# Kernel tuning notes

Hardware: AMD Instinct MI355X
Metric: run time of the kernel (lower is better)

Reference implementation:

```python
import jax, jax.numpy as jnp
import numpy as np

N_NODES = 1536
IN_FEATURES = 1433
N_HIDDEN = 64      # total across 8 heads -> 8 per head
N_HEADS = 8
N_CLASSES = 7
NEG_SLOPE = 0.2    # LeakyReLU slope in GATv2 layer


def setup_inputs() -> dict:
    key = jax.random.key(0)
    k_x, k_adj, k_w1, k_a1, k_w2, k_a2 = jax.random.split(key, 6)
    x = jax.random.normal(k_x, (N_NODES, IN_FEATURES), dtype=jnp.float32)
    adj = jax.random.uniform(k_adj, (N_NODES, N_NODES)) < 0.01
    adj = adj | jnp.eye(N_NODES, dtype=bool)
    adj_mat = adj[:, :, None]  # [n, n, 1]
    # layer 1 (share_weights=True -> one linear for l and r), attn vector shared across heads
    s1 = 1.0 / np.sqrt(IN_FEATURES)
    W1 = jax.random.uniform(k_w1, (IN_FEATURES, N_HIDDEN), minval=-s1, maxval=s1, dtype=jnp.float32)
    a1 = jax.random.uniform(k_a1, (N_HIDDEN // N_HEADS,), minval=-1.0, maxval=1.0, dtype=jnp.float32)
    # layer 2: 1 head, n_classes features, is_concat=False (mean over the single head)
    s2 = 1.0 / np.sqrt(N_HIDDEN)
    W2 = jax.random.uniform(k_w2, (N_HIDDEN, N_CLASSES), minval=-s2, maxval=s2, dtype=jnp.float32)
    a2 = jax.random.uniform(k_a2, (N_CLASSES,), minval=-1.0, maxval=1.0, dtype=jnp.float32)
    return {"x": x, "adj_mat": adj_mat, "W1": W1, "a1": a1, "W2": W2, "a2": a2}


def _gatv2_layer(h, adj, W, a, n_heads, is_concat):
    n = h.shape[0]
    g = (h @ W).reshape(n, n_heads, -1)              # shared weights: g_l == g_r == g
    # pairwise scores: e[i,j,h] = a . leaky_relu(g[j] + g[i])  (symmetric since weights shared)
    s = jax.nn.leaky_relu(g[:, None] + g[None, :], NEG_SLOPE)   # [n, n, heads, f]
    e = jnp.einsum('ijhf,f->ijh', s, a)                          # [n, n, heads]
    e = jnp.where(adj, e, -jnp.inf)                              # adj broadcasts [n,n,1]
    att = jax.nn.softmax(e, axis=1)                              # softmax over source nodes j
    out = jnp.einsum('ijh,jhf->ihf', att, g)                     # [n, heads, f]
    if is_concat:
        return out.reshape(n, -1)
    return out.mean(axis=1)


def reference(x, adj_mat, W1, a1, W2, a2):
    # dropout layers are identity in eval mode
    h = _gatv2_layer(x, adj_mat, W1, a1, N_HEADS, True)   # [n, n_hidden]
    h = jax.nn.elu(h)
    return _gatv2_layer(h, adj_mat, W2, a2, 1, False)     # [n, n_classes]
```

## Files before the change

### kernel.cpp

```cpp
#include <hip/hip_runtime.h>

#define N_NODES 1536
#define IN_F    1433
#define HID     64
#define NH      8
#define HF      8
#define NC      7
#define MAXN    64
#define GST     66
#define G1_BLOCKS 384
#define ROWS    4
#define XS_STRIDE 1440

__device__ __forceinline__ float waveAllMax(float v) {
#pragma unroll
    for (int o = 32; o > 0; o >>= 1) v = fmaxf(v, __shfl_xor(v, o, 64));
    return v;
}
__device__ __forceinline__ float waveAllSum(float v) {
#pragma unroll
    for (int o = 32; o > 0; o >>= 1) v += __shfl_xor(v, o, 64);
    return v;
}

__global__ __launch_bounds__(256) void k_front(const float* __restrict__ x,
                                               const float* __restrict__ W1,
                                               const unsigned int* __restrict__ adj,
                                               float* __restrict__ g1,
                                               int* __restrict__ cnt,
                                               int* __restrict__ nbr) {
    __shared__ float xs[ROWS * XS_STRIDE];
    __shared__ float red[4 * 256];
    __shared__ int lc;
    const int t = threadIdx.x;

    if (blockIdx.x < G1_BLOCKS) {
        const int i0 = blockIdx.x * ROWS;
        for (int r = 0; r < ROWS; ++r) {
            const float* xr = x + (size_t)(i0 + r) * IN_F;
            for (int k = t; k < XS_STRIDE; k += 256)
                xs[r * XS_STRIDE + k] = (k < IN_F) ? xr[k] : 0.f;
        }
        __syncthreads();
        const int j = t & 63, q = t >> 6;
        float acc[ROWS] = {0.f, 0.f, 0.f, 0.f};
        const int k0 = q * 360;
        for (int kb = k0; kb < k0 + 360; kb += 4) {
            float w[4];
#pragma unroll
            for (int u = 0; u < 4; ++u) {
                int k = kb + u;
                int kc = (k < IN_F) ? k : (IN_F - 1);
                w[u] = W1[(size_t)kc * HID + j];
            }
#pragma unroll
            for (int r = 0; r < ROWS; ++r) {
                float4 xv = *(const float4*)(xs + r * XS_STRIDE + kb);
                acc[r] += xv.x * w[0] + xv.y * w[1] + xv.z * w[2] + xv.w * w[3];
            }
        }
#pragma unroll
        for (int r = 0; r < ROWS; ++r) red[q * 256 + r * 64 + j] = acc[r];
        __syncthreads();
        float s = red[0 * 256 + t] + red[1 * 256 + t] + red[2 * 256 + t] + red[3 * 256 + t];
        g1[(size_t)(i0 + (t >> 6)) * HID + (t & 63)] = s;
    } else {
        const int i = blockIdx.x - G1_BLOCKS;
        if (t == 0) lc = 0;
        __syncthreads();
        const unsigned int* row = adj + (size_t)i * N_NODES;
        for (int j = t; j < N_NODES; j += 256) {
            if (row[j] != 0u) {
                int p = atomicAdd(&lc, 1);
                if (p < MAXN) nbr[i * MAXN + p] = j;
            }
        }
        __syncthreads();
        if (t == 0) {
            int n = (lc > MAXN) ? MAXN : lc;
            if (n == 0) { nbr[i * MAXN] = i; n = 1; }
            cnt[i] = n;
        }
    }
}

__global__ __launch_bounds__(64) void k_attn1(const float* __restrict__ g1,
                                              const int* __restrict__ cnt,
                                              const int* __restrict__ nbr,
                                              const float* __restrict__ a1,
                                              float* __restrict__ h1) {
    __shared__ float gis[HID];
    __shared__ float gj[MAXN * GST];
    __shared__ float es[NH * GST];
    const int i = blockIdx.x, t = threadIdx.x;
    const int n = cnt[i];

    gis[t] = g1[(size_t)i * HID + t];
    const int jn = nbr[i * MAXN + t];
    for (int l = 0; l < n; ++l) {
        int j = __shfl(jn, l, 64);
        gj[l * GST + t] = g1[(size_t)j * HID + t];
    }
    __syncthreads();

    float av[HF];
#pragma unroll
    for (int f = 0; f < HF; ++f) av[f] = a1[f];

    float sc[NH];
    if (t < n) {
#pragma unroll
        for (int h = 0; h < NH; ++h) {
            float s = 0.f;
#pragma unroll
            for (int f = 0; f < HF; ++f) {
                float v = gis[h * HF + f] + gj[t * GST + h * HF + f];
                v = (v >= 0.f) ? v : 0.2f * v;
                s += av[f] * v;
            }
            sc[h] = s;
        }
    } else {
#pragma unroll
        for (int h = 0; h < NH; ++h) sc[h] = -INFINITY;
    }

    float S[NH];
#pragma unroll
    for (int h = 0; h < NH; ++h) {
        float m = waveAllMax(sc[h]);
        float p = (t < n) ? __expf(sc[h] - m) : 0.f;
        es[h * GST + t] = p;
        S[h] = waveAllSum(p);
    }
    __syncthreads();

    const int h = t >> 3;
    float acc = 0.f;
    for (int l = 0; l < n; ++l)
        acc += es[h * GST + l] * gj[l * GST + t];
    acc /= S[h];
    h1[(size_t)i * HID + t] = (acc > 0.f) ? acc : (__expf(acc) - 1.f);
}

__global__ __launch_bounds__(64) void k_back(const float* __restrict__ h1,
                                             const float* __restrict__ W2,
                                             const float* __restrict__ a2,
                                             const int* __restrict__ cnt,
                                             const int* __restrict__ nbr,
                                             float* __restrict__ out) {
    __shared__ float hj[MAXN * GST];
    __shared__ float w2s[HID * NC];
    __shared__ float g2s[MAXN * 8];
    __shared__ float ps[MAXN];
    const int i = blockIdx.x, t = threadIdx.x;
    const int n = cnt[i];

    for (int k = t; k < HID * NC; k += 64) w2s[k] = W2[k];
    const int jn = nbr[i * MAXN + t];
    for (int l = 0; l < n; ++l) {
        int j = __shfl(jn, l, 64);
        hj[l * GST + t] = h1[(size_t)j * HID + t];
    }
    __syncthreads();

    if (t < n) {
#pragma unroll
        for (int c = 0; c < NC; ++c) {
            float s = 0.f;
            for (int f = 0; f < HID; ++f)
                s += hj[t * GST + f] * w2s[f * NC + c];
            g2s[t * 8 + c] = s;
        }
    }
    unsigned long long bal = __ballot(t < n && jn == i);
    int ls = (bal != 0ull) ? (__ffsll((long long)bal) - 1) : 0;
    __syncthreads();

    float scv;
    if (t < n) {
        float s = 0.f;
#pragma unroll
        for (int c = 0; c < NC; ++c) {
            float v = g2s[ls * 8 + c] + g2s[t * 8 + c];
            v = (v >= 0.f) ? v : 0.2f * v;
            s += a2[c] * v;
        }
        scv = s;
    } else scv = -INFINITY;

    float m = waveAllMax(scv);
    float p = (t < n) ? __expf(scv - m) : 0.f;
    ps[t] = p;
    float S = waveAllSum(p);
    __syncthreads();

    if (t < NC) {
        float acc = 0.f;
        for (int l = 0; l < n; ++l)
            acc += ps[l] * g2s[l * 8 + t];
        out[(size_t)i * NC + t] = acc / S;
    }
}

extern "C" void kernel_launch(void* const* d_in, const int* in_sizes, int n_in,
                              void* d_out, int out_size, void* d_ws, size_t ws_size,
                              hipStream_t stream) {
    (void)out_size; (void)ws_size;
    const void* px = nullptr; const void* padj = nullptr;
    const void* pW1 = nullptr; const void* pa1 = nullptr;
    const void* pW2 = nullptr; const void* pa2 = nullptr;
    for (int i = 0; i < n_in; ++i) {
        switch (in_sizes[i]) {
            case N_NODES * IN_F:    px   = d_in[i]; break;
            case N_NODES * N_NODES: padj = d_in[i]; break;
            case IN_F * HID:        pW1  = d_in[i]; break;
            case HF:                pa1  = d_in[i]; break;
            case HID * NC:          pW2  = d_in[i]; break;
            case NC:                pa2  = d_in[i]; break;
            default: break;
        }
    }
    if (!px && n_in > 0)   px   = d_in[0];
    if (!padj && n_in > 1) padj = d_in[1];
    if (!pW1 && n_in > 2)  pW1  = d_in[2];
    if (!pa1 && n_in > 3)  pa1  = d_in[3];
    if (!pW2 && n_in > 4)  pW2  = d_in[4];
    if (!pa2 && n_in > 5)  pa2  = d_in[5];

    char* w = (char*)d_ws;
    size_t off = 0;
    auto carve = [&](size_t bytes) -> char* {
        off = (off + 255) & ~(size_t)255;
        char* p = w + off; off += bytes; return p;
    };
    int*   cnt = (int*)  carve((size_t)N_NODES * 4);
    int*   nbr = (int*)  carve((size_t)N_NODES * MAXN * 4);
    float* g1  = (float*)carve((size_t)N_NODES * HID * 4);
    float* h1  = (float*)carve((size_t)N_NODES * HID * 4);

    float* outp = (float*)d_out;

    k_front<<<G1_BLOCKS + N_NODES, 256, 0, stream>>>((const float*)px, (const float*)pW1,
                                                     (const unsigned int*)padj, g1, cnt, nbr);
    k_attn1<<<N_NODES, 64, 0, stream>>>(g1, cnt, nbr, (const float*)pa1, h1);
    k_back<<<N_NODES, 64, 0, stream>>>(h1, (const float*)pW2, (const float*)pa2,
                                       cnt, nbr, outp);
}
```

Baseline: 122.7 us.

## Fuse three kernels into one cooperative persistent kernel with grid syncs

Merges the GEMM/compaction, layer-1 attention and layer-2 stages into a single cooperative kernel of 512 blocks that loops over work units and separates the stages with grid-wide barriers. Four wavefronts per block each handle one node in the attention stages, using slices of one shared LDS buffer. The aim is to remove two kernel launch gaps and their tail effects. In exchange, the grid-wide barriers add cost, a large LDS allocation limits occupancy, and the host now queries device attributes and occupancy on every call. The old three-kernel path stays as a fallback.

```diff
diff --git a/kernel.cpp b/kernel.cpp
--- a/kernel.cpp
+++ b/kernel.cpp
@@ -1,4 +1,7 @@
 #include <hip/hip_runtime.h>
+#include <hip/hip_cooperative_groups.h>
+
+namespace cg = cooperative_groups;
 
 #define N_NODES 1536
 #define IN_F    1433
@@ -11,6 +14,7 @@
 #define G1_BLOCKS 384
 #define ROWS    4
 #define XS_STRIDE 1440
+#define COOP_GRID 512
 
 __device__ __forceinline__ float waveAllMax(float v) {
 #pragma unroll
@@ -22,6 +26,180 @@
     for (int o = 32; o > 0; o >>= 1) v += __shfl_xor(v, o, 64);
     return v;
 }
+
+
+__device__ __forceinline__ void gemm1_unit(int u, const float* __restrict__ x,
+                                           const float* __restrict__ W1,
+                                           float* __restrict__ g1,
+                                           float* xs, float* red) {
+    const int t = threadIdx.x;
+    const int i0 = u * ROWS;
+    for (int r = 0; r < ROWS; ++r) {
+        const float* xr = x + (size_t)(i0 + r) * IN_F;
+        for (int k = t; k < XS_STRIDE; k += 256)
+            xs[r * XS_STRIDE + k] = (k < IN_F) ? xr[k] : 0.f;
+    }
+    __syncthreads();
+    const int j = t & 63, q = t >> 6;
+    float acc[ROWS] = {0.f, 0.f, 0.f, 0.f};
+    const int k0 = q * 360;
+    for (int kb = k0; kb < k0 + 360; kb += 4) {
+        float w[4];
+#pragma unroll
+        for (int u2 = 0; u2 < 4; ++u2) {
+            int k = kb + u2;
+            int kc = (k < IN_F) ? k : (IN_F - 1);
+            w[u2] = W1[(size_t)kc * HID + j];
+        }
+#pragma unroll
+        for (int r = 0; r < ROWS; ++r) {
+            float4 xv = *(const float4*)(xs + r * XS_STRIDE + kb);
+            acc[r] += xv.x * w[0] + xv.y * w[1] + xv.z * w[2] + xv.w * w[3];
+        }
+    }
+#pragma unroll
+    for (int r = 0; r < ROWS; ++r) red[q * 256 + r * 64 + j] = acc[r];
+    __syncthreads();
+    float s = red[0 * 256 + t] + red[1 * 256 + t] + red[2 * 256 + t] + red[3 * 256 + t];
+    g1[(size_t)(i0 + (t >> 6)) * HID + (t & 63)] = s;
+}
+
+__device__ __forceinline__ void compact_unit(int i, const unsigned int* __restrict__ adj,
+                                             int* __restrict__ cnt, int* __restrict__ nbr,
+                                             int* lc) {
+    const int t = threadIdx.x;
+    if (t == 0) *lc = 0;
+    __syncthreads();
+    const unsigned int* row = adj + (size_t)i * N_NODES;
+    for (int j = t; j < N_NODES; j += 256) {
+        if (row[j] != 0u) {
+            int p = atomicAdd(lc, 1);
+            if (p < MAXN) nbr[i * MAXN + p] = j;
+        }
+    }
+    __syncthreads();
+    if (t == 0) {
+        int n = (*lc > MAXN) ? MAXN : *lc;
+        if (n == 0) { nbr[i * MAXN] = i; n = 1; }
+        cnt[i] = n;
+    }
+}
+
+__device__ __forceinline__ void attn1_node(int i, int lane, const float* __restrict__ g1,
+                                           const int* __restrict__ cnt,
+                                           const int* __restrict__ nbr,
+                                           const float* __restrict__ a1,
+                                           float* __restrict__ h1, float* P) {
+    float* gis = P;
+    float* gj  = P + 64;
+    float* es  = P + 64 + MAXN * GST;
+    const int n = cnt[i];
+
+    gis[lane] = g1[(size_t)i * HID + lane];
+    const int jn = nbr[i * MAXN + lane];
+    for (int l = 0; l < n; ++l) {
+        int j = __shfl(jn, l, 64);
+        gj[l * GST + lane] = g1[(size_t)j * HID + lane];
+    }
+    __syncthreads();
+
+    float av[HF];
+#pragma unroll
+    for (int f = 0; f < HF; ++f) av[f] = a1[f];
+
+    float sc[NH];
+    if (lane < n) {
+#pragma unroll
+        for (int h = 0; h < NH; ++h) {
+            float s = 0.f;
+#pragma unroll
+            for (int f = 0; f < HF; ++f) {
+                float v = gis[h * HF + f] + gj[lane * GST + h * HF + f];
+                v = (v >= 0.f) ? v : 0.2f * v;
+                s += av[f] * v;
+            }
+            sc[h] = s;
+        }
+    } else {
+#pragma unroll
+        for (int h = 0; h < NH; ++h) sc[h] = -INFINITY;
+    }
+
+    float S[NH];
+#pragma unroll
+    for (int h = 0; h < NH; ++h) {
+        float m = waveAllMax(sc[h]);
+        float p = (lane < n) ? __expf(sc[h] - m) : 0.f;
+        es[h * GST + lane] = p;
+        S[h] = waveAllSum(p);
+    }
+    __syncthreads();
+
+    const int h = lane >> 3;
+    float acc = 0.f;
+    for (int l = 0; l < n; ++l)
+        acc += es[h * GST + l] * gj[l * GST + lane];
+    acc /= S[h];
+    h1[(size_t)i * HID + lane] = (acc > 0.f) ? acc : (__expf(acc) - 1.f);
+}
+
+__device__ __forceinline__ void back_node(int i, int lane, const float* __restrict__ h1,
+                                          const float* __restrict__ a2,
+                                          const int* __restrict__ cnt,
+                                          const int* __restrict__ nbr,
+                                          float* __restrict__ out,
+                                          float* Q, const float* w2s) {
+    float* hj  = Q;
+    float* g2s = Q + MAXN * GST;
+    float* ps  = Q + MAXN * GST + MAXN * 8;
+    const int n = cnt[i];
+
+    const int jn = nbr[i * MAXN + lane];
+    for (int l = 0; l < n; ++l) {
+        int j = __shfl(jn, l, 64);
+        hj[l * GST + lane] = h1[(size_t)j * HID + lane];
+    }
+    __syncthreads();
+
+    if (lane < n) {
+#pragma unroll
+        for (int c = 0; c < NC; ++c) {
+            float s = 0.f;
+            for (int f = 0; f < HID; ++f)
+                s += hj[lane * GST + f] * w2s[f * NC + c];
+            g2s[lane * 8 + c] = s;
+        }
+    }
+    unsigned long long bal = __ballot(lane < n && jn == i);
+    int ls = (bal != 0ull) ? (__ffsll((long long)bal) - 1) : 0;
+    __syncthreads();
+
+    float scv;
+    if (lane < n) {
+        float s = 0.f;
+#pragma unroll
+        for (int c = 0; c < NC; ++c) {
+            float v = g2s[ls * 8 + c] + g2s[lane * 8 + c];
+            v = (v >= 0.f) ? v : 0.2f * v;
+            s += a2[c] * v;
+        }
+        scv = s;
+    } else scv = -INFINITY;
+
+    float m = waveAllMax(scv);
+    float p = (lane < n) ? __expf(scv - m) : 0.f;
+    ps[lane] = p;
+    float S = waveAllSum(p);
+    __syncthreads();
+
+    if (lane < NC) {
+        float acc = 0.f;
+        for (int l = 0; l < n; ++l)
+            acc += ps[l] * g2s[l * 8 + lane];
+        out[(size_t)i * NC + lane] = acc / S;
+    }
+}
+
 
 __global__ __launch_bounds__(256) void k_front(const float* __restrict__ x,
                                                const float* __restrict__ W1,
@@ -32,56 +210,8 @@
     __shared__ float xs[ROWS * XS_STRIDE];
     __shared__ float red[4 * 256];
     __shared__ int lc;
-    const int t = threadIdx.x;
-
-    if (blockIdx.x < G1_BLOCKS) {
-        const int i0 = blockIdx.x * ROWS;
-        for (int r = 0; r < ROWS; ++r) {
-            const float* xr = x + (size_t)(i0 + r) * IN_F;
-            for (int k = t; k < XS_STRIDE; k += 256)
-                xs[r * XS_STRIDE + k] = (k < IN_F) ? xr[k] : 0.f;
-        }
-        __syncthreads();
-        const int j = t & 63, q = t >> 6;
-        float acc[ROWS] = {0.f, 0.f, 0.f, 0.f};
-        const int k0 = q * 360;
-        for (int kb = k0; kb < k0 + 360; kb += 4) {
-            float w[4];
-#pragma unroll
-            for (int u = 0; u < 4; ++u) {
-                int k = kb + u;
-                int kc = (k < IN_F) ? k : (IN_F - 1);
-                w[u] = W1[(size_t)kc * HID + j];
-            }
-#pragma unroll
-            for (int r = 0; r < ROWS; ++r) {
-                float4 xv = *(const float4*)(xs + r * XS_STRIDE + kb);
-                acc[r] += xv.x * w[0] + xv.y * w[1] + xv.z * w[2] + xv.w * w[3];
-            }
-        }
-#pragma unroll
-        for (int r = 0; r < ROWS; ++r) red[q * 256 + r * 64 + j] = acc[r];
-        __syncthreads();
-        float s = red[0 * 256 + t] + red[1 * 256 + t] + red[2 * 256 + t] + red[3 * 256 + t];
-        g1[(size_t)(i0 + (t >> 6)) * HID + (t & 63)] = s;
-    } else {
-        const int i = blockIdx.x - G1_BLOCKS;
-        if (t == 0) lc = 0;
-        __syncthreads();
-        const unsigned int* row = adj + (size_t)i * N_NODES;
-        for (int j = t; j < N_NODES; j += 256) {
-            if (row[j] != 0u) {
-                int p = atomicAdd(&lc, 1);
-                if (p < MAXN) nbr[i * MAXN + p] = j;
-            }
-        }
-        __syncthreads();
-        if (t == 0) {
-            int n = (lc > MAXN) ? MAXN : lc;
-            if (n == 0) { nbr[i * MAXN] = i; n = 1; }
-            cnt[i] = n;
-        }
-    }
+    if (blockIdx.x < G1_BLOCKS) gemm1_unit(blockIdx.x, x, W1, g1, xs, red);
+    else                        compact_unit(blockIdx.x - G1_BLOCKS, adj, cnt, nbr, &lc);
 }
 
 __global__ __launch_bounds__(64) void k_attn1(const float* __restrict__ g1,
@@ -89,58 +219,8 @@
                                               const int* __restrict__ nbr,
                                               const float* __restrict__ a1,
                                               float* __restrict__ h1) {
-    __shared__ float gis[HID];
-    __shared__ float gj[MAXN * GST];
-    __shared__ float es[NH * GST];
-    const int i = blockIdx.x, t = threadIdx.x;
-    const int n = cnt[i];
-
-    gis[t] = g1[(size_t)i * HID + t];
-    const int jn = nbr[i * MAXN + t];
-    for (int l = 0; l < n; ++l) {
-        int j = __shfl(jn, l, 64);
-        gj[l * GST + t] = g1[(size_t)j * HID + t];
-    }
-    __syncthreads();
-
-    float av[HF];
-#pragma unroll
-    for (int f = 0; f < HF; ++f) av[f] = a1[f];
-
-    float sc[NH];
-    if (t < n) {
-#pragma unroll
-        for (int h = 0; h < NH; ++h) {
-            float s = 0.f;
-#pragma unroll
-            for (int f = 0; f < HF; ++f) {
-                float v = gis[h * HF + f] + gj[t * GST + h * HF + f];
-                v = (v >= 0.f) ? v : 0.2f * v;
-                s += av[f] * v;
-            }
-            sc[h] = s;
-        }
-    } else {
-#pragma unroll
-        for (int h = 0; h < NH; ++h) sc[h] = -INFINITY;
-    }
-
-    float S[NH];
-#pragma unroll
-    for (int h = 0; h < NH; ++h) {
-        float m = waveAllMax(sc[h]);
-        float p = (t < n) ? __expf(sc[h] - m) : 0.f;
-        es[h * GST + t] = p;
-        S[h] = waveAllSum(p);
-    }
-    __syncthreads();
-
-    const int h = t >> 3;
-    float acc = 0.f;
-    for (int l = 0; l < n; ++l)
-        acc += es[h * GST + l] * gj[l * GST + t];
-    acc /= S[h];
-    h1[(size_t)i * HID + t] = (acc > 0.f) ? acc : (__expf(acc) - 1.f);
+    __shared__ float P[64 + MAXN * GST + NH * GST];
+    attn1_node(blockIdx.x, threadIdx.x, g1, cnt, nbr, a1, h1, P);
 }
 
 __global__ __launch_bounds__(64) void k_back(const float* __restrict__ h1,
@@ -149,58 +229,45 @@
                                              const int* __restrict__ cnt,
                                              const int* __restrict__ nbr,
                                              float* __restrict__ out) {
-    __shared__ float hj[MAXN * GST];
+    __shared__ float Q[MAXN * GST + MAXN * 8 + 64];
     __shared__ float w2s[HID * NC];
-    __shared__ float g2s[MAXN * 8];
-    __shared__ float ps[MAXN];
-    const int i = blockIdx.x, t = threadIdx.x;
-    const int n = cnt[i];
-
-    for (int k = t; k < HID * NC; k += 64) w2s[k] = W2[k];
-    const int jn = nbr[i * MAXN + t];
-    for (int l = 0; l < n; ++l) {
-        int j = __shfl(jn, l, 64);
-        hj[l * GST + t] = h1[(size_t)j * HID + t];
-    }
-    __syncthreads();
-
-    if (t < n) {
-#pragma unroll
-        for (int c = 0; c < NC; ++c) {
-            float s = 0.f;
-            for (int f = 0; f < HID; ++f)
-                s += hj[t * GST + f] * w2s[f * NC + c];
-            g2s[t * 8 + c] = s;
-        }
-    }
-    unsigned long long bal = __ballot(t < n && jn == i);
-    int ls = (bal != 0ull) ? (__ffsll((long long)bal) - 1) : 0;
-    __syncthreads();
-
-    float scv;
-    if (t < n) {
-        float s = 0.f;
-#pragma unroll
-        for (int c = 0; c < NC; ++c) {
-            float v = g2s[ls * 8 + c] + g2s[t * 8 + c];
-            v = (v >= 0.f) ? v : 0.2f * v;
-            s += a2[c] * v;
-        }
-        scv = s;
-    } else scv = -INFINITY;
-
-    float m = waveAllMax(scv);
-    float p = (t < n) ? __expf(scv - m) : 0.f;
-    ps[t] = p;
-    float S = waveAllSum(p);
-    __syncthreads();
-
-    if (t < NC) {
-        float acc = 0.f;
-        for (int l = 0; l < n; ++l)
-            acc += ps[l] * g2s[l * 8 + t];
-        out[(size_t)i * NC + t] = acc / S;
-    }
+    for (int k = threadIdx.x; k < HID * NC; k += 64) w2s[k] = W2[k];
+    back_node(blockIdx.x, threadIdx.x, h1, a2, cnt, nbr, out, Q, w2s);
+}
+
+__global__ __launch_bounds__(256) void k_all(const float* __restrict__ x,
+                                             const float* __restrict__ W1,
+                                             const unsigned int* __restrict__ adj,
+                                             const float* __restrict__ a1,
+                                             const float* __restrict__ W2,
+                                             const float* __restrict__ a2,
+                                             int* __restrict__ cnt,
+                                             int* __restrict__ nbr,
+                                             float* __restrict__ g1,
+                                             float* __restrict__ h1,
+                                             float* __restrict__ out) {
+    __shared__ float lds[19648];
+    __shared__ int lc;
+    const int t = threadIdx.x;
+    cg::grid_group grid = cg::this_grid();
+
+    for (int u = blockIdx.x; u < G1_BLOCKS + N_NODES; u += gridDim.x) {
+        if (u < G1_BLOCKS) gemm1_unit(u, x, W1, g1, lds, lds + ROWS * XS_STRIDE);
+        else               compact_unit(u - G1_BLOCKS, adj, cnt, nbr, &lc);
+        __syncthreads();
+    }
+    grid.sync();
+
+    const int w = t >> 6, lane = t & 63;
+    for (int i = blockIdx.x * 4 + w; i < N_NODES; i += gridDim.x * 4)
+        attn1_node(i, lane, g1, cnt, nbr, a1, h1, lds + w * 4816);
+    grid.sync();
+
+    float* w2s = lds + 4 * 4800;
+    for (int k = t; k < HID * NC; k += 256) w2s[k] = W2[k];
+    __syncthreads();
+    for (int i = blockIdx.x * 4 + w; i < N_NODES; i += gridDim.x * 4)
+        back_node(i, lane, h1, a2, cnt, nbr, out, lds + w * 4800, w2s);
 }
 
 extern "C" void kernel_launch(void* const* d_in, const int* in_sizes, int n_in,
@@ -239,11 +306,33 @@
     float* g1  = (float*)carve((size_t)N_NODES * HID * 4);
     float* h1  = (float*)carve((size_t)N_NODES * HID * 4);
 
-    float* outp = (float*)d_out;
-
-    k_front<<<G1_BLOCKS + N_NODES, 256, 0, stream>>>((const float*)px, (const float*)pW1,
-                                                     (const unsigned int*)padj, g1, cnt, nbr);
-    k_attn1<<<N_NODES, 64, 0, stream>>>(g1, cnt, nbr, (const float*)pa1, h1);
-    k_back<<<N_NODES, 64, 0, stream>>>(h1, (const float*)pW2, (const float*)pa2,
-                                       cnt, nbr, outp);
-}
+    const float* xf         = (const float*)px;
+    const float* W1f        = (const float*)pW1;
+    const unsigned int* adw = (const unsigned int*)padj;
+    const float* a1f        = (const float*)pa1;
+    const float* W2f        = (const float*)pW2;
+    const float* a2f        = (const float*)pa2;
+    float* outp             = (float*)d_out;
+
+    int dev = 0; (void)hipGetDevice(&dev);
+    int coop = 0;
+    (void)hipDeviceGetAttribute(&coop, hipDeviceAttributeCooperativeLaunch, dev);
+    int maxb = 0;
+    if (coop)
+        (void)hipOccupancyMaxActiveBlocksPerMultiprocessor(&maxb, (const void*)k_all, 256, 0);
+
+    bool done = false;
+    if (coop && maxb >= 2) {
+        void* args[] = { (void*)&xf, (void*)&W1f, (void*)&adw, (void*)&a1f,
+                         (void*)&W2f, (void*)&a2f, (void*)&cnt, (void*)&nbr,
+                         (void*)&g1, (void*)&h1, (void*)&outp };
+        hipError_t e = hipLaunchCooperativeKernel((const void*)k_all, dim3(COOP_GRID),
+                                                  dim3(256), args, 0, stream);
+        done = (e == hipSuccess);
+    }
+    if (!done) {
+        k_front<<<G1_BLOCKS + N_NODES, 256, 0, stream>>>(xf, W1f, adw, g1, cnt, nbr);
+        k_attn1<<<N_NODES, 64, 0, stream>>>(g1, cnt, nbr, a1f, h1);
+        k_back<<<N_NODES, 64, 0, stream>>>(h1, W2f, a2f, cnt, nbr, outp);
+    }
+}
```

New measurement: 132.0 us. 1.08x slower.
